# Kernel tuning notes

Measured on AMD Instinct MI355X. Metric: run time of the kernel, lower is better.

The kernel has to match this reference:

```python
import jax, jax.numpy as jnp
import numpy as np

IMG = 1024.0
POOL = 7
STRIDES = (4, 8, 16, 32)  # levels P2..P5
STDS = jnp.array([0.1, 0.1, 0.2, 0.2], dtype=jnp.float32)  # RCNN_TARGET_STDS


def delta2bbox(rois, deltas):
    # rois: [N,4] (y1,x1,y2,x2) pixels; deltas: [N,4]
    d = deltas * STDS  # means are zero
    y1, x1, y2, x2 = rois[:, 0], rois[:, 1], rois[:, 2], rois[:, 3]
    h = y2 - y1
    w = x2 - x1
    cy = y1 + 0.5 * h + d[:, 0] * h
    cx = x1 + 0.5 * w + d[:, 1] * w
    h = h * jnp.exp(d[:, 2])
    w = w * jnp.exp(d[:, 3])
    b = jnp.stack([cy - 0.5 * h, cx - 0.5 * w, cy + 0.5 * h, cx + 0.5 * w], axis=1)
    return jnp.clip(b, 0.0, IMG)


def crop_level(feat, rois, stride):
    # feat: [H,W,C]; bilinear 7x7 crop (crop_and_resize style)
    H, W, _ = feat.shape
    s = rois / stride
    grid = (jnp.arange(POOL, dtype=jnp.float32) + 0.5) / POOL
    ys = s[:, 0:1] + grid[None, :] * (s[:, 2:3] - s[:, 0:1])  # [N,7]
    xs = s[:, 1:2] + grid[None, :] * (s[:, 3:4] - s[:, 1:2])  # [N,7]
    y0f = jnp.clip(jnp.floor(ys), 0.0, H - 1)
    x0f = jnp.clip(jnp.floor(xs), 0.0, W - 1)
    y0 = y0f.astype(jnp.int32)
    x0 = x0f.astype(jnp.int32)
    y1 = jnp.minimum(y0 + 1, H - 1)
    x1 = jnp.minimum(x0 + 1, W - 1)
    wy = jnp.clip(ys - y0f, 0.0, 1.0)[:, :, None, None]  # [N,7,1,1]
    wx = jnp.clip(xs - x0f, 0.0, 1.0)[:, None, :, None]  # [N,1,7,1]
    g = lambda yi, xi: feat[yi[:, :, None], xi[:, None, :]]  # [N,7,7,C]
    return (g(y0, x0) * (1 - wy) * (1 - wx) + g(y0, x1) * (1 - wy) * wx
            + g(y1, x0) * wy * (1 - wx) + g(y1, x1) * wy * wx)


def pyramid_roi_align(feats, rois):
    h = rois[:, 2] - rois[:, 0]
    w = rois[:, 3] - rois[:, 1]
    lvl = jnp.floor(4.0 + jnp.log2(jnp.sqrt(jnp.maximum(h * w, 1e-6)) / 224.0))
    lvl = jnp.clip(lvl, 2.0, 5.0).astype(jnp.int32)
    pooled = 0.0
    for i, (feat, stride) in enumerate(zip(feats, STRIDES)):
        mask = (lvl == i + 2).astype(feat.dtype)[:, None, None, None]
        pooled = pooled + crop_level(feat, rois, stride) * mask
    return pooled  # [N,7,7,C]


def bbox_head(pooled, i, fc1_w, fc1_b, fc2_w, fc2_b, cls_w, cls_b, reg_w, reg_b):
    n = pooled.shape[0]
    x = pooled.reshape(n, -1)
    h1 = jax.nn.relu(x @ fc1_w[i] + fc1_b[i])
    h2 = jax.nn.relu(h1 @ fc2_w[i] + fc2_b[i])
    logits = h2 @ cls_w[i] + cls_b[i]
    probs = jax.nn.softmax(logits, axis=-1)
    deltas = h2 @ reg_w[i] + reg_b[i]
    return logits, probs, deltas


def setup_inputs() -> dict:
    key = jax.random.key(0)
    ks = jax.random.split(key, 16)
    d = {}
    for j, (name, shp) in enumerate([("P2", (1, 256, 256, 256)), ("P3", (1, 128, 128, 256)),
                                     ("P4", (1, 64, 64, 256)), ("P5", (1, 32, 32, 256))]):
        d[name] = jax.random.normal(ks[j], shp, dtype=jnp.float32)
    N = 1000
    u = jax.random.uniform(ks[4], (N, 4))
    hh = 16.0 * 2.0 ** (u[:, 0] * 5.0)  # box sizes 16..512 px, spans all pyramid levels
    ww = 16.0 * 2.0 ** (u[:, 1] * 5.0)
    y1 = u[:, 2] * (IMG - hh)
    x1 = u[:, 3] * (IMG - ww)
    d["rois"] = jnp.stack([y1, x1, y1 + hh, x1 + ww], axis=1)
    d["fc1_w"] = jax.random.normal(ks[5], (3, 12544, 1024), dtype=jnp.float32) * 0.01
    d["fc1_b"] = jnp.zeros((3, 1024), jnp.float32)
    d["fc2_w"] = jax.random.normal(ks[6], (3, 1024, 1024), dtype=jnp.float32) * 0.02
    d["fc2_b"] = jnp.zeros((3, 1024), jnp.float32)
    d["cls_w"] = jax.random.normal(ks[7], (3, 1024, 81), dtype=jnp.float32) * 0.02
    d["cls_b"] = jnp.zeros((3, 81), jnp.float32)
    d["reg_w"] = jax.random.normal(ks[8], (3, 1024, 4), dtype=jnp.float32) * 0.01
    d["reg_b"] = jnp.zeros((3, 4), jnp.float32)
    return d


def reference(P2, P3, P4, P5, rois, fc1_w, fc1_b, fc2_w, fc2_b, cls_w, cls_b, reg_w, reg_b):
    feats = [P2[0], P3[0], P4[0], P5[0]]
    params = (fc1_w, fc1_b, fc2_w, fc2_b, cls_w, cls_b, reg_w, reg_b)
    r = rois
    probs3 = None
    pooled = None
    for i in range(3):
        pooled = pyramid_roi_align(feats, r)
        _, probs3, deltas = bbox_head(pooled, i, *params)
        if i < 2:
            r = delta2bbox(r, deltas)
    # test-time ensemble: heads 1 and 2 re-applied to final pooled regions
    _, probs1, _ = bbox_head(pooled, 0, *params)
    _, probs2, _ = bbox_head(pooled, 1, *params)
    return (probs3 + probs1 + probs2) / 3.0
```

## Files before the change

kernel.cpp:

```cpp
#include <hip/hip_runtime.h>


#define BM 128
#define BN 128
#define BK 32
#define K1 12544
#define MPAD 1024
#define NROI 1000

typedef __bf16 bf16_t;
typedef bf16_t bf16x8 __attribute__((ext_vector_type(8)));
typedef float f32x4 __attribute__((ext_vector_type(4)));

__device__ __forceinline__ unsigned short f2bf(float x) {
  unsigned u = __float_as_uint(x);
  return (unsigned short)((u + 0x7fffu + ((u >> 16) & 1u)) >> 16);
}
__device__ __forceinline__ float bf2f(unsigned short h) {
  return __uint_as_float(((unsigned)h) << 16);
}

__device__ __forceinline__ void gld_lds16(const void* g, void* l) {
  __builtin_amdgcn_global_load_lds(
      (__attribute__((address_space(1))) void*)g,
      (__attribute__((address_space(3))) void*)l, 16, 0, 0);
}

template <bool SPLIT>
__global__ __launch_bounds__(256, 4)
void gemm_bf16(const unsigned short* __restrict__ Ah,
               const unsigned short* __restrict__ Al,
               long long strideA_head,
               const unsigned short* __restrict__ Bh,
               const unsigned short* __restrict__ Bl,
               long long strideB_head,
               float* __restrict__ Cpart,
               int Nh, int K, int kcSteps)
{
  __shared__ __align__(16) unsigned short sAh[BM * BK];
  __shared__ __align__(16) unsigned short sBh[BN * BK];
  __shared__ __align__(16) unsigned short sAl[SPLIT ? BM * BK : 8];
  __shared__ __align__(16) unsigned short sBl[SPLIT ? BN * BK : 8];

  const int t = threadIdx.x;
  const int ntile = Nh / BN;
  const int bm = blockIdx.x / ntile;
  const int bn = blockIdx.x % ntile;
  const int s = blockIdx.y;
  const int h = blockIdx.z;
  const int H = gridDim.z;

  const unsigned short* Ab = Ah + (size_t)h * strideA_head + (size_t)bm * BM * K;
  const unsigned short* Bb = Bh + (size_t)h * strideB_head + (size_t)bn * BN * K;
  const unsigned short* Alb = SPLIT ? (Al + (size_t)h * strideA_head + (size_t)bm * BM * K) : (const unsigned short*)0;
  const unsigned short* Blb = SPLIT ? (Bl + (size_t)h * strideB_head + (size_t)bn * BN * K) : (const unsigned short*)0;

  int k0 = s * kcSteps * BK;
  int k1 = min(K, k0 + kcSteps * BK);

  const int srow = t >> 2;
  const int gsw = ((t & 3) ^ ((srow >> 1) & 3)) * 8;
  const int lane = t & 63;
  const int wv = t >> 6;
  const int wm = (wv >> 1) * 64;
  const int wn = (wv & 1) * 64;
  const int lr = lane & 15;
  const int q = lane >> 4;
  const int sw = (lr >> 1) & 3;
  const int cA = (q ^ sw) * 8;

  f32x4 acc[4][4];
  const f32x4 z = {0.f, 0.f, 0.f, 0.f};
#pragma unroll
  for (int i = 0; i < 4; ++i)
#pragma unroll
    for (int j = 0; j < 4; ++j) acc[i][j] = z;

  for (int kk = k0; kk < k1; kk += BK) {
#pragma unroll
    for (int j = 0; j < 2; ++j) {
      int row = j * 64 + srow;
      gld_lds16(Ab + (size_t)row * K + kk + gsw, (char*)sAh + j * 4096 + t * 16);
      gld_lds16(Bb + (size_t)row * K + kk + gsw, (char*)sBh + j * 4096 + t * 16);
      if constexpr (SPLIT) {
        gld_lds16(Alb + (size_t)row * K + kk + gsw, (char*)sAl + j * 4096 + t * 16);
        gld_lds16(Blb + (size_t)row * K + kk + gsw, (char*)sBl + j * 4096 + t * 16);
      }
    }
    __syncthreads();

    bf16x8 af[4], bfr[4];
#pragma unroll
    for (int i = 0; i < 4; ++i) af[i] = *(const bf16x8*)&sAh[(wm + i * 16 + lr) * BK + cA];
#pragma unroll
    for (int j = 0; j < 4; ++j) bfr[j] = *(const bf16x8*)&sBh[(wn + j * 16 + lr) * BK + cA];
#pragma unroll
    for (int i = 0; i < 4; ++i)
#pragma unroll
      for (int j = 0; j < 4; ++j)
        acc[i][j] = __builtin_amdgcn_mfma_f32_16x16x32_bf16(af[i], bfr[j], acc[i][j], 0, 0, 0);

    if constexpr (SPLIT) {
      bf16x8 al[4], bl[4];
#pragma unroll
      for (int i = 0; i < 4; ++i) al[i] = *(const bf16x8*)&sAl[(wm + i * 16 + lr) * BK + cA];
#pragma unroll
      for (int j = 0; j < 4; ++j) bl[j] = *(const bf16x8*)&sBl[(wn + j * 16 + lr) * BK + cA];
#pragma unroll
      for (int i = 0; i < 4; ++i)
#pragma unroll
        for (int j = 0; j < 4; ++j) {
          acc[i][j] = __builtin_amdgcn_mfma_f32_16x16x32_bf16(af[i], bl[j], acc[i][j], 0, 0, 0);
          acc[i][j] = __builtin_amdgcn_mfma_f32_16x16x32_bf16(al[i], bfr[j], acc[i][j], 0, 0, 0);
        }
    }
    __syncthreads();
  }

  float* Cb = Cpart + ((size_t)(s * H + h) * MPAD + (size_t)bm * BM) * Nh + (size_t)bn * BN;
#pragma unroll
  for (int i = 0; i < 4; ++i)
#pragma unroll
    for (int j = 0; j < 4; ++j)
#pragma unroll
      for (int r = 0; r < 4; ++r) {
        int m = wm + i * 16 + q * 4 + r;
        int n = wn + j * 16 + lr;
        Cb[(size_t)m * Nh + n] = acc[i][j][r];
      }
}

__global__ void epilogue_kernel(const float* __restrict__ Cpart, int S, int H, int Nh,
                                const float* __restrict__ bias, int nbias,
                                unsigned short* __restrict__ ohi,
                                unsigned short* __restrict__ olo,
                                float* __restrict__ of32, int flags)
{
  size_t idx = (size_t)blockIdx.x * 256 + threadIdx.x;
  size_t total = (size_t)H * MPAD * Nh;
  if (idx >= total) return;
  int n = (int)(idx % Nh);
  int h = (int)(idx / ((size_t)MPAD * Nh));
  float v = 0.f;
  for (int s = 0; s < S; ++s) v += Cpart[(size_t)s * total + idx];
  if (n < nbias) v += bias[(size_t)h * nbias + n];
  if (flags & 1) v = fmaxf(v, 0.f);
  if (flags & 8) of32[idx] = v;
  if (flags & 2) {
    unsigned short hi = f2bf(v);
    ohi[idx] = hi;
    if (flags & 4) olo[idx] = f2bf(v - bf2f(hi));
  }
}

__global__ void transpose_convert(const float* __restrict__ W,
                                  unsigned short* __restrict__ Thi,
                                  unsigned short* __restrict__ Tlo,
                                  int K, int N, int loHeads)
{
  __shared__ float tile[32][33];
  int kb = blockIdx.x * 32;
  int nb = blockIdx.y * 32;
  int h = blockIdx.z;
  const float* Wb = W + (size_t)h * K * N;
  int tc = threadIdx.x & 31;
  int tr = threadIdx.x >> 5;
#pragma unroll
  for (int j = 0; j < 4; ++j) {
    int kk = tr + j * 8;
    tile[kk][tc] = Wb[(size_t)(kb + kk) * N + nb + tc];
  }
  __syncthreads();
  size_t ob = (size_t)h * N * K;
  bool wlo = h < loHeads;
#pragma unroll
  for (int j = 0; j < 4; ++j) {
    int nn = tr + j * 8;
    float v = tile[tc][nn];
    unsigned short hi = f2bf(v);
    size_t o = ob + (size_t)(nb + nn) * K + kb + tc;
    Thi[o] = hi;
    if (wlo) Tlo[o] = f2bf(v - bf2f(hi));
  }
}

__global__ void transpose_cls(const float* __restrict__ W, unsigned short* __restrict__ T)
{
  int n = blockIdx.x, h = blockIdx.y, t = threadIdx.x;
  size_t ob = ((size_t)h * 128 + n) * 1024;
  if (n < 81) {
    for (int k = t; k < 1024; k += 256)
      T[ob + k] = f2bf(W[((size_t)h * 1024 + k) * 81 + n]);
  } else {
    for (int k = t; k < 1024; k += 256) T[ob + k] = 0;
  }
}

__global__ void roi_align_kernel(const float* __restrict__ rois,
                                 const float* __restrict__ P2, const float* __restrict__ P3,
                                 const float* __restrict__ P4, const float* __restrict__ P5,
                                 unsigned short* __restrict__ phi,
                                 unsigned short* __restrict__ plo, int writeLo)
{
  int m = blockIdx.x;
  int c = threadIdx.x;
  const float* rp = rois + m * 4;
  float y1 = rp[0], x1 = rp[1], y2 = rp[2], x2 = rp[3];
  float hh = y2 - y1, ww = x2 - x1;
  float a = sqrtf(fmaxf(hh * ww, 1e-6f)) / 224.0f;
  float lvl = floorf(4.0f + log2f(a));
  lvl = fminf(fmaxf(lvl, 2.0f), 5.0f);
  int i = (int)lvl - 2;
  const float* f = (i == 0) ? P2 : (i == 1) ? P3 : (i == 2) ? P4 : P5;
  int H = 256 >> i;
  float stride = (float)(4 << i);
  float sy1 = y1 / stride, sx1 = x1 / stride;
  float dy = y2 / stride - sy1, dx = x2 / stride - sx1;
  size_t base = (size_t)m * K1 + c;
  for (int p = 0; p < 49; ++p) {
    int py = p / 7, px = p % 7;
    float ys = sy1 + ((py + 0.5f) / 7.0f) * dy;
    float xs = sx1 + ((px + 0.5f) / 7.0f) * dx;
    float y0f = fminf(fmaxf(floorf(ys), 0.0f), (float)(H - 1));
    float x0f = fminf(fmaxf(floorf(xs), 0.0f), (float)(H - 1));
    int y0 = (int)y0f, x0 = (int)x0f;
    int y1i = min(y0 + 1, H - 1), x1i = min(x0 + 1, H - 1);
    float wy = fminf(fmaxf(ys - y0f, 0.0f), 1.0f);
    float wx = fminf(fmaxf(xs - x0f, 0.0f), 1.0f);
    const float* r0 = f + (size_t)y0 * H * 256;
    const float* r1 = f + (size_t)y1i * H * 256;
    float v00 = r0[(size_t)x0 * 256 + c];
    float v01 = r0[(size_t)x1i * 256 + c];
    float v10 = r1[(size_t)x0 * 256 + c];
    float v11 = r1[(size_t)x1i * 256 + c];
    float v = v00 * (1.f - wy) * (1.f - wx) + v01 * (1.f - wy) * wx +
              v10 * wy * (1.f - wx) + v11 * wy * wx;
    unsigned short hi = f2bf(v);
    phi[base + p * 256] = hi;
    if (writeLo) plo[base + p * 256] = f2bf(v - bf2f(hi));
  }
}

__global__ void reg_delta_kernel(const unsigned short* __restrict__ h2h,
                                 const unsigned short* __restrict__ h2l,
                                 const float* __restrict__ rw, const float* __restrict__ rb,
                                 const float* __restrict__ rin, float* __restrict__ rout)
{
  int m = blockIdx.x, t = threadIdx.x;
  float s0 = 0, s1 = 0, s2 = 0, s3 = 0;
  const unsigned short* hr = h2h + (size_t)m * 1024;
  const unsigned short* lr = h2l + (size_t)m * 1024;
  for (int k = t; k < 1024; k += 256) {
    float hv = bf2f(hr[k]) + bf2f(lr[k]);
    const float* w = rw + (size_t)k * 4;
    s0 += hv * w[0]; s1 += hv * w[1]; s2 += hv * w[2]; s3 += hv * w[3];
  }
#pragma unroll
  for (int o = 32; o > 0; o >>= 1) {
    s0 += __shfl_xor(s0, o, 64);
    s1 += __shfl_xor(s1, o, 64);
    s2 += __shfl_xor(s2, o, 64);
    s3 += __shfl_xor(s3, o, 64);
  }
  __shared__ float part[4][4];
  int w = t >> 6;
  if ((t & 63) == 0) { part[w][0] = s0; part[w][1] = s1; part[w][2] = s2; part[w][3] = s3; }
  __syncthreads();
  if (t == 0) {
    float d0 = (part[0][0] + part[1][0] + part[2][0] + part[3][0] + rb[0]) * 0.1f;
    float d1 = (part[0][1] + part[1][1] + part[2][1] + part[3][1] + rb[1]) * 0.1f;
    float d2 = (part[0][2] + part[1][2] + part[2][2] + part[3][2] + rb[2]) * 0.2f;
    float d3 = (part[0][3] + part[1][3] + part[2][3] + part[3][3] + rb[3]) * 0.2f;
    const float* r = rin + m * 4;
    float y1 = r[0], x1 = r[1], y2 = r[2], x2 = r[3];
    float h = y2 - y1, wd = x2 - x1;
    float cy = y1 + 0.5f * h + d0 * h;
    float cx = x1 + 0.5f * wd + d1 * wd;
    float nh = h * expf(d2);
    float nw = wd * expf(d3);
    float* ro = rout + m * 4;
    ro[0] = fminf(fmaxf(cy - 0.5f * nh, 0.f), 1024.f);
    ro[1] = fminf(fmaxf(cx - 0.5f * nw, 0.f), 1024.f);
    ro[2] = fminf(fmaxf(cy + 0.5f * nh, 0.f), 1024.f);
    ro[3] = fminf(fmaxf(cx + 0.5f * nw, 0.f), 1024.f);
  }
}

__global__ void softmax_avg_kernel(const float* __restrict__ logits, float* __restrict__ out)
{
  int m = blockIdx.x, t = threadIdx.x;
  __shared__ float sh[128];
  float pacc = 0.0f;
  for (int h = 0; h < 3; ++h) {
    float x = (t < 81) ? logits[((size_t)(h * MPAD + m)) * 128 + t] : -3.0e38f;
    sh[t] = x; __syncthreads();
    for (int o = 64; o > 0; o >>= 1) { if (t < o) sh[t] = fmaxf(sh[t], sh[t + o]); __syncthreads(); }
    float mx = sh[0]; __syncthreads();
    float e = (t < 81) ? expf(x - mx) : 0.0f;
    sh[t] = e; __syncthreads();
    for (int o = 64; o > 0; o >>= 1) { if (t < o) sh[t] += sh[t + o]; __syncthreads(); }
    float sum = sh[0]; __syncthreads();
    pacc += e / sum;
  }
  if (t < 81) out[(size_t)m * 81 + t] = pacc / 3.0f;
}

extern "C" void kernel_launch(void* const* d_in, const int* in_sizes, int n_in,
                              void* d_out, int out_size, void* d_ws, size_t ws_size,
                              hipStream_t stream)
{
  const float* P2 = (const float*)d_in[0];
  const float* P3 = (const float*)d_in[1];
  const float* P4 = (const float*)d_in[2];
  const float* P5 = (const float*)d_in[3];
  const float* rois = (const float*)d_in[4];
  const float* fc1_w = (const float*)d_in[5];
  const float* fc1_b = (const float*)d_in[6];
  const float* fc2_w = (const float*)d_in[7];
  const float* fc2_b = (const float*)d_in[8];
  const float* cls_w = (const float*)d_in[9];
  const float* cls_b = (const float*)d_in[10];
  const float* reg_w = (const float*)d_in[11];
  const float* reg_b = (const float*)d_in[12];
  float* out = (float*)d_out;

  char* ws = (char*)d_ws;
  size_t off = 0;
  auto alloc = [&](size_t b) -> char* {
    char* p = ws + off;
    off = (off + b + 255) & ~(size_t)255;
    return p;
  };
  unsigned short* w1t_hi = (unsigned short*)alloc(3ull * 1024 * K1 * 2);
  unsigned short* w1t_lo = (unsigned short*)alloc(2ull * 1024 * K1 * 2);
  unsigned short* w2t_hi = (unsigned short*)alloc(3ull * 1024 * 1024 * 2);
  unsigned short* w2t_lo = (unsigned short*)alloc(2ull * 1024 * 1024 * 2);
  unsigned short* w3t    = (unsigned short*)alloc(3ull * 128 * 1024 * 2);
  unsigned short* phi    = (unsigned short*)alloc((size_t)MPAD * K1 * 2);
  unsigned short* plo    = (unsigned short*)alloc((size_t)MPAD * K1 * 2);
  unsigned short* h1_hi  = (unsigned short*)alloc(3ull * MPAD * 1024 * 2);
  unsigned short* h1_lo  = (unsigned short*)alloc((size_t)MPAD * 1024 * 2);
  unsigned short* h2_hi  = (unsigned short*)alloc(3ull * MPAD * 1024 * 2);
  unsigned short* h2_lo  = (unsigned short*)alloc((size_t)MPAD * 1024 * 2);
  float* logitsb         = (float*)alloc(3ull * MPAD * 128 * 4);
  float* r1              = (float*)alloc(16384);
  float* r2              = (float*)alloc(16384);

  const size_t SLAB = (size_t)MPAD * 1024 * 4;
  size_t remain = (ws_size > off) ? (ws_size - off) : 0;
  int S01 = (int)(remain / SLAB);
  if (S01 > 8) S01 = 8;
  if (S01 < 1) S01 = 1;
  float* cpart01 = (float*)(ws + off);
  float* cpart2 = (float*)w1t_lo;

  const int fc1Steps01 = (392 + S01 - 1) / S01;
  const int fc2Steps01 = (32 + S01 - 1) / S01;

  const long long hs1 = (long long)1024 * K1;
  const long long hs2 = (long long)1024 * 1024;

  dim3 b256(256);

  hipLaunchKernelGGL(transpose_convert, dim3(K1 / 32, 32, 3), b256, 0, stream,
                     fc1_w, w1t_hi, w1t_lo, K1, 1024, 2);
  hipLaunchKernelGGL(transpose_convert, dim3(32, 32, 3), b256, 0, stream,
                     fc2_w, w2t_hi, w2t_lo, 1024, 1024, 2);
  hipLaunchKernelGGL(transpose_cls, dim3(128, 3), b256, 0, stream, cls_w, w3t);
  hipMemsetAsync(phi + (size_t)NROI * K1, 0, (size_t)(MPAD - NROI) * K1 * 2, stream);
  hipMemsetAsync(plo + (size_t)NROI * K1, 0, (size_t)(MPAD - NROI) * K1 * 2, stream);

  for (int st = 0; st < 2; ++st) {
    const float* rin = (st == 0) ? rois : r1;
    float* rout = (st == 0) ? r1 : r2;
    hipLaunchKernelGGL(roi_align_kernel, dim3(NROI), b256, 0, stream,
                       rin, P2, P3, P4, P5, phi, plo, 1);
    hipLaunchKernelGGL((gemm_bf16<true>), dim3(64, S01, 1), b256, 0, stream,
                       phi, plo, 0LL,
                       w1t_hi + (size_t)st * hs1, w1t_lo + (size_t)st * hs1, 0LL,
                       cpart01, 1024, K1, fc1Steps01);
    hipLaunchKernelGGL(epilogue_kernel, dim3(4096), b256, 0, stream,
                       cpart01, S01, 1, 1024, fc1_b + st * 1024, 1024,
                       h1_hi, h1_lo, (float*)0, 1 | 2 | 4);
    hipLaunchKernelGGL((gemm_bf16<true>), dim3(64, S01, 1), b256, 0, stream,
                       h1_hi, h1_lo, 0LL,
                       w2t_hi + (size_t)st * hs2, w2t_lo + (size_t)st * hs2, 0LL,
                       cpart01, 1024, 1024, fc2Steps01);
    hipLaunchKernelGGL(epilogue_kernel, dim3(4096), b256, 0, stream,
                       cpart01, S01, 1, 1024, fc2_b + st * 1024, 1024,
                       h2_hi, h2_lo, (float*)0, 1 | 2 | 4);
    hipLaunchKernelGGL(reg_delta_kernel, dim3(NROI), b256, 0, stream,
                       h2_hi, h2_lo, reg_w + (size_t)st * 1024 * 4, reg_b + st * 4,
                       rin, rout);
  }

  hipLaunchKernelGGL(roi_align_kernel, dim3(NROI), b256, 0, stream,
                     r2, P2, P3, P4, P5, phi, plo, 0);
  hipLaunchKernelGGL((gemm_bf16<false>), dim3(64, 4, 3), b256, 0, stream,
                     phi, (const unsigned short*)0, 0LL,
                     w1t_hi, (const unsigned short*)0, hs1,
                     cpart2, 1024, K1, 98);
  hipLaunchKernelGGL(epilogue_kernel, dim3(12288), b256, 0, stream,
                     cpart2, 4, 3, 1024, fc1_b, 1024,
                     h1_hi, (unsigned short*)0, (float*)0, 1 | 2);
  hipLaunchKernelGGL((gemm_bf16<false>), dim3(64, 4, 3), b256, 0, stream,
                     h1_hi, (const unsigned short*)0, hs2,
                     w2t_hi, (const unsigned short*)0, hs2,
                     cpart2, 1024, 1024, 8);
  hipLaunchKernelGGL(epilogue_kernel, dim3(12288), b256, 0, stream,
                     cpart2, 4, 3, 1024, fc2_b, 1024,
                     h2_hi, (unsigned short*)0, (float*)0, 1 | 2);
  hipLaunchKernelGGL((gemm_bf16<false>), dim3(8, 8, 3), b256, 0, stream,
                     h2_hi, (const unsigned short*)0, hs2,
                     w3t, (const unsigned short*)0, (long long)128 * 1024,
                     cpart2, 128, 1024, 4);
  hipLaunchKernelGGL(epilogue_kernel, dim3(1536), b256, 0, stream,
                     cpart2, 8, 3, 128, cls_b, 81,
                     (unsigned short*)0, (unsigned short*)0, logitsb, 8);
  hipLaunchKernelGGL(softmax_avg_kernel, dim3(NROI), dim3(128), 0, stream,
                     logitsb, out);
}
```

Before: 894.7 us.

## Vectorize transpose and ROI align, raise split-K factors from workspace size

The weight transpose-convert kernel now stages 256 K-values per block and writes 4-wide vectorized bf16 stores. ROI align loads and stores two channels per thread, with two sample-point groups per block. The split-K factor for the fc1 GEMMs is derived from the available workspace, up to 16 in the first two stages and up to 8 in the final stage, to give more parallelism to the long-K GEMM. In exchange the epilogue has to sum more partial buffers.

```diff
diff --git a/kernel.cpp b/kernel.cpp
--- a/kernel.cpp
+++ b/kernel.cpp
@@ -11,6 +11,9 @@
 typedef __bf16 bf16_t;
 typedef bf16_t bf16x8 __attribute__((ext_vector_type(8)));
 typedef float f32x4 __attribute__((ext_vector_type(4)));
+typedef float f32x2 __attribute__((ext_vector_type(2)));
+typedef unsigned short u16x4 __attribute__((ext_vector_type(4)));
+typedef unsigned short u16x2 __attribute__((ext_vector_type(2)));
 
 __device__ __forceinline__ unsigned short f2bf(float x) {
   unsigned u = __float_as_uint(x);
@@ -153,34 +156,43 @@
   }
 }
 
-__global__ void transpose_convert(const float* __restrict__ W,
-                                  unsigned short* __restrict__ Thi,
-                                  unsigned short* __restrict__ Tlo,
-                                  int K, int N, int loHeads)
-{
-  __shared__ float tile[32][33];
-  int kb = blockIdx.x * 32;
+__global__ __launch_bounds__(256)
+void transpose_convert(const float* __restrict__ W,
+                       unsigned short* __restrict__ Thi,
+                       unsigned short* __restrict__ Tlo,
+                       int K, int N, int loHeads)
+{
+  __shared__ float tile[32][260];
+  int kb = blockIdx.x * 256;
   int nb = blockIdx.y * 32;
   int h = blockIdx.z;
-  const float* Wb = W + (size_t)h * K * N;
-  int tc = threadIdx.x & 31;
-  int tr = threadIdx.x >> 5;
-#pragma unroll
-  for (int j = 0; j < 4; ++j) {
-    int kk = tr + j * 8;
-    tile[kk][tc] = Wb[(size_t)(kb + kk) * N + nb + tc];
+  const float* Wb = W + (size_t)h * K * N + (size_t)kb * N + nb;
+  int tn = threadIdx.x & 31;
+  int tk = threadIdx.x >> 5;
+#pragma unroll
+  for (int i = 0; i < 32; ++i) {
+    int k = tk + i * 8;
+    tile[tn][k] = Wb[(size_t)k * N + tn];
   }
   __syncthreads();
-  size_t ob = (size_t)h * N * K;
   bool wlo = h < loHeads;
-#pragma unroll
-  for (int j = 0; j < 4; ++j) {
-    int nn = tr + j * 8;
-    float v = tile[tc][nn];
-    unsigned short hi = f2bf(v);
-    size_t o = ob + (size_t)(nb + nn) * K + kb + tc;
-    Thi[o] = hi;
-    if (wlo) Tlo[o] = f2bf(v - bf2f(hi));
+  int l = threadIdx.x & 63;
+  int ng = threadIdx.x >> 6;
+  size_t ob = (size_t)h * N * K + (size_t)nb * K + kb;
+#pragma unroll
+  for (int i = 0; i < 8; ++i) {
+    int n = ng + i * 4;
+    f32x4 v = *(const f32x4*)&tile[n][4 * l];
+    u16x4 hi;
+#pragma unroll
+    for (int j = 0; j < 4; ++j) hi[j] = f2bf(v[j]);
+    *(u16x4*)&Thi[ob + (size_t)n * K + 4 * l] = hi;
+    if (wlo) {
+      u16x4 lo;
+#pragma unroll
+      for (int j = 0; j < 4; ++j) lo[j] = f2bf(v[j] - bf2f(hi[j]));
+      *(u16x4*)&Tlo[ob + (size_t)n * K + 4 * l] = lo;
+    }
   }
 }
 
@@ -203,7 +215,9 @@
                                  unsigned short* __restrict__ plo, int writeLo)
 {
   int m = blockIdx.x;
-  int c = threadIdx.x;
+  int t = threadIdx.x;
+  int c = (t & 127) * 2;
+  int pg = t >> 7;
   const float* rp = rois + m * 4;
   float y1 = rp[0], x1 = rp[1], y2 = rp[2], x2 = rp[3];
   float hh = y2 - y1, ww = x2 - x1;
@@ -217,7 +231,7 @@
   float sy1 = y1 / stride, sx1 = x1 / stride;
   float dy = y2 / stride - sy1, dx = x2 / stride - sx1;
   size_t base = (size_t)m * K1 + c;
-  for (int p = 0; p < 49; ++p) {
+  for (int p = pg; p < 49; p += 2) {
     int py = p / 7, px = p % 7;
     float ys = sy1 + ((py + 0.5f) / 7.0f) * dy;
     float xs = sx1 + ((px + 0.5f) / 7.0f) * dx;
@@ -227,17 +241,22 @@
     int y1i = min(y0 + 1, H - 1), x1i = min(x0 + 1, H - 1);
     float wy = fminf(fmaxf(ys - y0f, 0.0f), 1.0f);
     float wx = fminf(fmaxf(xs - x0f, 0.0f), 1.0f);
-    const float* r0 = f + (size_t)y0 * H * 256;
-    const float* r1 = f + (size_t)y1i * H * 256;
-    float v00 = r0[(size_t)x0 * 256 + c];
-    float v01 = r0[(size_t)x1i * 256 + c];
-    float v10 = r1[(size_t)x0 * 256 + c];
-    float v11 = r1[(size_t)x1i * 256 + c];
-    float v = v00 * (1.f - wy) * (1.f - wx) + v01 * (1.f - wy) * wx +
-              v10 * wy * (1.f - wx) + v11 * wy * wx;
-    unsigned short hi = f2bf(v);
-    phi[base + p * 256] = hi;
-    if (writeLo) plo[base + p * 256] = f2bf(v - bf2f(hi));
+    f32x2 v00 = *(const f32x2*)(f + ((size_t)y0 * H + x0) * 256 + c);
+    f32x2 v01 = *(const f32x2*)(f + ((size_t)y0 * H + x1i) * 256 + c);
+    f32x2 v10 = *(const f32x2*)(f + ((size_t)y1i * H + x0) * 256 + c);
+    f32x2 v11 = *(const f32x2*)(f + ((size_t)y1i * H + x1i) * 256 + c);
+    float w00 = (1.f - wy) * (1.f - wx), w01 = (1.f - wy) * wx;
+    float w10 = wy * (1.f - wx), w11 = wy * wx;
+    f32x2 v = v00 * w00 + v01 * w01 + v10 * w10 + v11 * w11;
+    u16x2 hi;
+    hi[0] = f2bf(v[0]); hi[1] = f2bf(v[1]);
+    *(u16x2*)&phi[base + p * 256] = hi;
+    if (writeLo) {
+      u16x2 lo;
+      lo[0] = f2bf(v[0] - bf2f(hi[0]));
+      lo[1] = f2bf(v[1] - bf2f(hi[1]));
+      *(u16x2*)&plo[base + p * 256] = lo;
+    }
   }
 }
 
@@ -332,7 +351,6 @@
     return p;
   };
   unsigned short* w1t_hi = (unsigned short*)alloc(3ull * 1024 * K1 * 2);
-  unsigned short* w1t_lo = (unsigned short*)alloc(2ull * 1024 * K1 * 2);
   unsigned short* w2t_hi = (unsigned short*)alloc(3ull * 1024 * 1024 * 2);
   unsigned short* w2t_lo = (unsigned short*)alloc(2ull * 1024 * 1024 * 2);
   unsigned short* w3t    = (unsigned short*)alloc(3ull * 128 * 1024 * 2);
@@ -345,26 +363,35 @@
   float* logitsb         = (float*)alloc(3ull * MPAD * 128 * 4);
   float* r1              = (float*)alloc(16384);
   float* r2              = (float*)alloc(16384);
+  const size_t w1lo_bytes = 2ull * 1024 * K1 * 2;
+  unsigned short* w1t_lo = (unsigned short*)alloc(w1lo_bytes);
 
   const size_t SLAB = (size_t)MPAD * 1024 * 4;
-  size_t remain = (ws_size > off) ? (ws_size - off) : 0;
-  int S01 = (int)(remain / SLAB);
-  if (S01 > 8) S01 = 8;
+  size_t tail = (ws_size > off) ? (ws_size - off) : 0;
+
+  int S01 = (int)(tail / SLAB);
+  if (S01 > 16) S01 = 16;
   if (S01 < 1) S01 = 1;
+  int S01b = S01 > 8 ? 8 : S01;
   float* cpart01 = (float*)(ws + off);
+  size_t cap2 = w1lo_bytes + tail;
+  int S2 = (int)(cap2 / (3 * SLAB));
+  if (S2 > 8) S2 = 8;
+  if (S2 < 1) S2 = 1;
   float* cpart2 = (float*)w1t_lo;
 
   const int fc1Steps01 = (392 + S01 - 1) / S01;
-  const int fc2Steps01 = (32 + S01 - 1) / S01;
+  const int fc2Steps01 = (32 + S01b - 1) / S01b;
+  const int fc1Steps2 = (392 + S2 - 1) / S2;
 
   const long long hs1 = (long long)1024 * K1;
   const long long hs2 = (long long)1024 * 1024;
 
   dim3 b256(256);
 
-  hipLaunchKernelGGL(transpose_convert, dim3(K1 / 32, 32, 3), b256, 0, stream,
+  hipLaunchKernelGGL(transpose_convert, dim3(K1 / 256, 32, 3), b256, 0, stream,
                      fc1_w, w1t_hi, w1t_lo, K1, 1024, 2);
-  hipLaunchKernelGGL(transpose_convert, dim3(32, 32, 3), b256, 0, stream,
+  hipLaunchKernelGGL(transpose_convert, dim3(4, 32, 3), b256, 0, stream,
                      fc2_w, w2t_hi, w2t_lo, 1024, 1024, 2);
   hipLaunchKernelGGL(transpose_cls, dim3(128, 3), b256, 0, stream, cls_w, w3t);
   hipMemsetAsync(phi + (size_t)NROI * K1, 0, (size_t)(MPAD - NROI) * K1 * 2, stream);
@@ -382,12 +409,12 @@
     hipLaunchKernelGGL(epilogue_kernel, dim3(4096), b256, 0, stream,
                        cpart01, S01, 1, 1024, fc1_b + st * 1024, 1024,
                        h1_hi, h1_lo, (float*)0, 1 | 2 | 4);
-    hipLaunchKernelGGL((gemm_bf16<true>), dim3(64, S01, 1), b256, 0, stream,
+    hipLaunchKernelGGL((gemm_bf16<true>), dim3(64, S01b, 1), b256, 0, stream,
                        h1_hi, h1_lo, 0LL,
                        w2t_hi + (size_t)st * hs2, w2t_lo + (size_t)st * hs2, 0LL,
                        cpart01, 1024, 1024, fc2Steps01);
     hipLaunchKernelGGL(epilogue_kernel, dim3(4096), b256, 0, stream,
-                       cpart01, S01, 1, 1024, fc2_b + st * 1024, 1024,
+                       cpart01, S01b, 1, 1024, fc2_b + st * 1024, 1024,
                        h2_hi, h2_lo, (float*)0, 1 | 2 | 4);
     hipLaunchKernelGGL(reg_delta_kernel, dim3(NROI), b256, 0, stream,
                        h2_hi, h2_lo, reg_w + (size_t)st * 1024 * 4, reg_b + st * 4,
@@ -396,19 +423,20 @@
 
   hipLaunchKernelGGL(roi_align_kernel, dim3(NROI), b256, 0, stream,
                      r2, P2, P3, P4, P5, phi, plo, 0);
-  hipLaunchKernelGGL((gemm_bf16<false>), dim3(64, 4, 3), b256, 0, stream,
+  hipLaunchKernelGGL((gemm_bf16<false>), dim3(64, S2, 3), b256, 0, stream,
                      phi, (const unsigned short*)0, 0LL,
                      w1t_hi, (const unsigned short*)0, hs1,
-                     cpart2, 1024, K1, 98);
+                     cpart2, 1024, K1, fc1Steps2);
   hipLaunchKernelGGL(epilogue_kernel, dim3(12288), b256, 0, stream,
-                     cpart2, 4, 3, 1024, fc1_b, 1024,
+                     cpart2, S2, 3, 1024, fc1_b, 1024,
                      h1_hi, (unsigned short*)0, (float*)0, 1 | 2);
-  hipLaunchKernelGGL((gemm_bf16<false>), dim3(64, 4, 3), b256, 0, stream,
+  int S2f = S2 > 8 ? 8 : S2;
+  hipLaunchKernelGGL((gemm_bf16<false>), dim3(64, S2f, 3), b256, 0, stream,
                      h1_hi, (const unsigned short*)0, hs2,
                      w2t_hi, (const unsigned short*)0, hs2,
-                     cpart2, 1024, 1024, 8);
+                     cpart2, 1024, 1024, (32 + S2f - 1) / S2f);
   hipLaunchKernelGGL(epilogue_kernel, dim3(12288), b256, 0, stream,
-                     cpart2, 4, 3, 1024, fc2_b, 1024,
+                     cpart2, S2f, 3, 1024, fc2_b, 1024,
                      h2_hi, (unsigned short*)0, (float*)0, 1 | 2);
   hipLaunchKernelGGL((gemm_bf16<false>), dim3(8, 8, 3), b256, 0, stream,
                      h2_hi, (const unsigned short*)0, hs2,
```

New measurement: 941.0 us. 5.2% more time.
